# Kernel tuning notes

Measured on AMD Instinct MI355X. Metric: run time of the kernel, lower is better.

The kernel has to match this reference:

```python
import jax, jax.numpy as jnp
import numpy as np

T, N, D = 64, 40, 4
H, R, K = 256, 64, 2
E = N * (N - 1)


def _xavier(key, shape):
    std = (2.0 / (shape[0] + shape[1])) ** 0.5
    return (std * jax.random.normal(key, shape)).astype(jnp.float32)


def setup_inputs() -> dict:
    ks = iter(jax.random.split(jax.random.key(0), 40))
    send, recv = np.where(np.ones((N, N)) - np.eye(N))  # fully-connected directed graph, E = N*(N-1)
    p = {}
    p['inputs'] = jax.random.normal(next(ks), (1, T, N, D), dtype=jnp.float32)
    p['node_masks'] = jnp.ones((1, T, N), dtype=jnp.float32)
    p['send_edges'] = jnp.asarray(send, dtype=jnp.int32)
    p['recv_edges'] = jnp.asarray(recv, dtype=jnp.int32)
    for name, nin in (('mlp1', D), ('mlp2', 2 * H), ('mlp3', H), ('mlp4', 3 * H)):
        p[name + '_W1'] = _xavier(next(ks), (H, nin))
        p[name + '_b1'] = jnp.full((H,), 0.1, jnp.float32)
        p[name + '_W2'] = _xavier(next(ks), (H, H))
        p[name + '_b2'] = jnp.full((H,), 0.1, jnp.float32)
    s = float(1.0 / np.sqrt(R))
    for nm in ('fwd', 'rev'):
        p[nm + '_Wih'] = jax.random.uniform(next(ks), (4 * R, H), jnp.float32, -s, s)
        p[nm + '_Whh'] = jax.random.uniform(next(ks), (4 * R, R), jnp.float32, -s, s)
        p[nm + '_bih'] = jnp.zeros((4 * R,), jnp.float32)
        p[nm + '_bhh'] = jnp.zeros((4 * R,), jnp.float32)
    p['enc_W'] = _xavier(next(ks), (K, 2 * R))
    p['enc_b'] = jnp.full((K,), 0.1, jnp.float32)
    p['prior_W'] = _xavier(next(ks), (K, R))
    p['prior_b'] = jnp.full((K,), 0.1, jnp.float32)
    return p


def _mlp(x, W1, b1, W2, b2):
    # RefNRIMLP in eval mode with no_bn=True: elu(fc2(elu(fc1(x))))
    return jax.nn.elu(jax.nn.elu(x @ W1.T + b1) @ W2.T + b2)


def _lstm(xs, Wih, Whh, bih, bhh):
    # xs: [T, E, H] -> hidden states [T, E, R]; PyTorch LSTM gate order i, f, g, o
    def step(carry, xt):
        h, c = carry
        g = xt @ Wih.T + bih + h @ Whh.T + bhh
        i, f, gg, o = jnp.split(g, 4, axis=-1)
        c = jax.nn.sigmoid(f) * c + jax.nn.sigmoid(i) * jnp.tanh(gg)
        h = jax.nn.sigmoid(o) * jnp.tanh(c)
        return (h, c), h
    Rh = Whh.shape[1]
    init = (jnp.zeros((xs.shape[1], Rh), xs.dtype), jnp.zeros((xs.shape[1], Rh), xs.dtype))
    _, hs = jax.lax.scan(step, init, xs)
    return hs


def _encode(inputs, send, recv,
            m1W1, m1b1, m1W2, m1b2, m2W1, m2b1, m2W2, m2b2,
            m3W1, m3b1, m3W2, m3b2, m4W1, m4b1, m4W2, m4b2,
            fWih, fWhh, fbih, fbhh, rWih, rWhh, rbih, rbhh,
            encW, encb, priW, prib):
    x = inputs[0]                                                  # [T, N, D]
    h = _mlp(x, m1W1, m1b1, m1W2, m1b2)                            # [T, N, H]
    e = jnp.concatenate([h[:, send], h[:, recv]], axis=-1)         # node2edge gather [T, E, 2H]
    e = _mlp(e, m2W1, m2b1, m2W2, m2b2)                            # [T, E, H]
    skip = e
    n = jnp.zeros((x.shape[0], x.shape[1], e.shape[-1]), e.dtype)
    n = n.at[:, recv].add(e)                                       # edge2node scatter-add (index_add_)
    n = _mlp(n, m3W1, m3b1, m3W2, m3b2)                            # [T, N, H]
    e = jnp.concatenate([n[:, send], n[:, recv], skip], axis=-1)   # [T, E, 3H]
    e = _mlp(e, m4W1, m4b1, m4W2, m4b2)                            # per-edge features over time [T, E, H]
    fwd_h = _lstm(e, fWih, fWhh, fbih, fbhh)                       # [T, E, R]
    rev_h = _lstm(e[::-1], rWih, rWhh, rbih, rbhh)[::-1]           # [T, E, R]
    prior = fwd_h @ priW.T + prib                                  # [T, E, K]
    enc = jnp.concatenate([fwd_h, rev_h], axis=-1) @ encW.T + encb # [T, E, K]
    return jnp.concatenate([prior, enc], axis=-1)                  # [T, E, 2K]


def reference(inputs, node_masks, send_edges, recv_edges,
              mlp1_W1, mlp1_b1, mlp1_W2, mlp1_b2,
              mlp2_W1, mlp2_b1, mlp2_W2, mlp2_b2,
              mlp3_W1, mlp3_b1, mlp3_W2, mlp3_b2,
              mlp4_W1, mlp4_b1, mlp4_W2, mlp4_b2,
              fwd_Wih, fwd_Whh, fwd_bih, fwd_bhh,
              rev_Wih, rev_Whh, rev_bih, rev_bhh,
              enc_W, enc_b, prior_W, prior_b):
    del node_masks  # all nodes present -> static fully-connected graph each step
    return _encode(inputs, send_edges, recv_edges,
                   mlp1_W1, mlp1_b1, mlp1_W2, mlp1_b2,
                   mlp2_W1, mlp2_b1, mlp2_W2, mlp2_b2,
                   mlp3_W1, mlp3_b1, mlp3_W2, mlp3_b2,
                   mlp4_W1, mlp4_b1, mlp4_W2, mlp4_b2,
                   fwd_Wih, fwd_Whh, fwd_bih, fwd_bhh,
                   rev_Wih, rev_Whh, rev_bih, rev_bhh,
                   enc_W, enc_b, prior_W, prior_b)
```

## Files before the change

kernel.cpp:

```cpp
#include <hip/hip_runtime.h>
#include <math.h>

#define T_ 64
#define N_ 40
#define D_ 4
#define H_ 256
#define R_ 64
#define E_ 1560
#define TE_ (T_*E_)
#define TN_ (T_*N_)

typedef unsigned short us;
typedef short short8 __attribute__((ext_vector_type(8)));
typedef float f32x4 __attribute__((ext_vector_type(4)));

__device__ __forceinline__ float elu_f(float x){ return x > 0.f ? x : (__expf(x) - 1.f); }
__device__ __forceinline__ float sig_f(float x){ return 1.f/(1.f+__expf(-x)); }
__device__ __forceinline__ float tanh_f(float x){ return 2.f/(1.f+__expf(-2.f*x)) - 1.f; }
__device__ __forceinline__ float dot4(float4 a, float4 b){ return a.x*b.x + a.y*b.y + a.z*b.z + a.w*b.w; }

__device__ __forceinline__ float bf2f(us u){ return __uint_as_float(((unsigned int)u) << 16); }
__device__ __forceinline__ us f2bf(float f){
    unsigned int u = __float_as_uint(f);
    u += 0x7FFFu + ((u >> 16) & 1u);
    return (us)(u >> 16);
}
__device__ __forceinline__ float4 ld4f(const float* p){ return *(const float4*)p; }
__device__ __forceinline__ float4 ld4f(const us* p){
    ushort4 v = *(const ushort4*)p;
    return make_float4(bf2f(v.x), bf2f(v.y), bf2f(v.z), bf2f(v.w));
}
__device__ __forceinline__ void st4f(float* p, float4 v){ *(float4*)p = v; }
__device__ __forceinline__ void st4f(us* p, float4 v){
    ushort4 o; o.x = f2bf(v.x); o.y = f2bf(v.y); o.z = f2bf(v.z); o.w = f2bf(v.w);
    *(ushort4*)p = o;
}

__device__ __forceinline__ void gld16(void* lds, const void* g){
    __builtin_amdgcn_global_load_lds((const __attribute__((address_space(1))) unsigned int*)g,
                                     (__attribute__((address_space(3))) unsigned int*)lds,
                                     16, 0, 0);
}

__device__ __forceinline__ void wsplit1(const float* W, us* hi, us* lo, int i){
    const float w = W[i];
    const us h = f2bf(w);
    hi[i] = h;
    lo[i] = f2bf(w - bf2f(h));
}

__device__ __forceinline__ void wsplitF(const float* __restrict__ W, int stride, int colOff,
                                        us* hi, us* lo, int i){
    const int jj   = i & 7;
    const int lane = (i >> 3) & 63;
    const int mt   = (i >> 9) & 1;
    const int k    = (i >> 10) & 7;
    const int fh   = i >> 13;
    const int R = fh * 32 + mt * 16 + (lane & 15);
    const int K = k * 32 + (lane >> 4) * 8 + jj;
    const float w = W[(size_t)R * stride + colOff + K];
    const us h = f2bf(w);
    hi[i] = h;
    lo[i] = f2bf(w - bf2f(h));
}

__global__ __launch_bounds__(256)
void wsplit_all(const float* __restrict__ s0, us* h0, us* l0,
                const float* __restrict__ s1, us* h1, us* l1,
                const float* __restrict__ s2, us* h2, us* l2,
                const float* __restrict__ s3, us* h3, us* l3,
                const float* __restrict__ s4, us* h4, us* l4,
                const float* __restrict__ s5, us* h5, us* l5,
                const float* __restrict__ s6, us* h6, us* l6)
{
    int i = blockIdx.x * 256 + threadIdx.x;
    if (i < 65536) { wsplitF(s0, 256,   0, h0, l0, i); return; } i -= 65536;
    if (i < 65536) { wsplitF(s1, 768, 512, h1, l1, i); return; } i -= 65536;
    if (i < 65536) { wsplitF(s2, 256,   0, h2, l2, i); return; } i -= 65536;
    if (i < 65536) { wsplitF(s3, 256,   0, h3, l3, i); return; } i -= 65536;
    if (i < 65536) { wsplitF(s4, 256,   0, h4, l4, i); return; } i -= 65536;
    if (i < 16384) { wsplit1(s5, h5, l5, i); return; } i -= 16384;
    wsplit1(s6, h6, l6, i);
}

__global__ __launch_bounds__(256)
void mlp1_kernel(const float* __restrict__ x,
                 const float* __restrict__ W1, const float* __restrict__ b1,
                 const float* __restrict__ W2, const float* __restrict__ b2,
                 us* __restrict__ hout)
{
    __shared__ float xs[8][4];
    __shared__ float h1[8][256];
    const int tid = threadIdx.x;
    const int r0  = blockIdx.x * 8;

    if (tid < 32) xs[tid >> 2][tid & 3] = x[r0 * 4 + tid];
    __syncthreads();

    const float4 w1 = *(const float4*)&W1[tid * 4];
    const float bb1 = b1[tid];
    #pragma unroll
    for (int row = 0; row < 8; ++row) {
        float v = bb1 + xs[row][0]*w1.x + xs[row][1]*w1.y + xs[row][2]*w1.z + xs[row][3]*w1.w;
        h1[row][tid] = elu_f(v);
    }
    __syncthreads();

    float acc[8];
    const float bb2 = b2[tid];
    #pragma unroll
    for (int row = 0; row < 8; ++row) acc[row] = bb2;
    const float* w2row = W2 + (size_t)tid * 256;
    for (int k4 = 0; k4 < 64; ++k4) {
        const float4 w = *(const float4*)&w2row[k4 * 4];
        #pragma unroll
        for (int row = 0; row < 8; ++row) {
            const float4 hh = *(const float4*)&h1[row][k4 * 4];
            acc[row] += dot4(hh, w);
        }
    }
    #pragma unroll
    for (int row = 0; row < 8; ++row)
        hout[(size_t)(r0 + row) * 256 + tid] = f2bf(elu_f(acc[row]));
}

__global__ __launch_bounds__(256)
void node_proj(const us* __restrict__ A, const float* __restrict__ W,
               int wstride, float* __restrict__ P)
{
    __shared__ float As[16][64];
    __shared__ float Ws[16][64];

    const int tid  = threadIdx.x;
    const int am   = tid >> 2;
    const int gm   = blockIdx.x * 64 + am;
    const int part = blockIdx.y >> 2;
    const int wq   = blockIdx.y & 3;

    const us* aptr = A + (size_t)gm * 256;
    const float* wptr = W + (size_t)(wq * 64 + am) * wstride + part * 256;

    const int tx = tid & 15, ty = tid >> 4;
    float acc[4][4] = {};

    for (int k0 = 0; k0 < 256; k0 += 16) {
        const float4 a4 = ld4f(aptr + k0 + (tid & 3) * 4);
        const float4 w4 = *(const float4*)(wptr + k0 + (tid & 3) * 4);

        __syncthreads();
        const int ak = (tid & 3) * 4;
        As[ak+0][am] = a4.x; As[ak+1][am] = a4.y; As[ak+2][am] = a4.z; As[ak+3][am] = a4.w;
        Ws[ak+0][am] = w4.x; Ws[ak+1][am] = w4.y; Ws[ak+2][am] = w4.z; Ws[ak+3][am] = w4.w;
        __syncthreads();

        #pragma unroll
        for (int kq = 0; kq < 16; ++kq) {
            const float4 av = *(const float4*)&As[kq][ty * 4];
            const float4 wv = *(const float4*)&Ws[kq][tx * 4];
            const float a_[4] = {av.x, av.y, av.z, av.w};
            const float w_[4] = {wv.x, wv.y, wv.z, wv.w};
            #pragma unroll
            for (int i = 0; i < 4; ++i)
                #pragma unroll
                for (int j = 0; j < 4; ++j)
                    acc[i][j] += a_[i] * w_[j];
        }
    }

    const int gn = part * 256 + wq * 64 + tx * 4;
    #pragma unroll
    for (int i = 0; i < 4; ++i) {
        const int row = blockIdx.x * 64 + ty * 4 + i;
        float4 o;
        o.x = acc[i][0]; o.y = acc[i][1]; o.z = acc[i][2]; o.w = acc[i][3];
        *(float4*)(P + (size_t)row * 512 + gn) = o;
    }
}

__global__ __launch_bounds__(256)
void edge_gather_elu(const float* __restrict__ P, const float* __restrict__ b1,
                     const int* __restrict__ send, const int* __restrict__ recv,
                     us* __restrict__ out)
{
    const int tid = threadIdx.x;
    const int r   = blockIdx.x * 4 + (tid >> 6);
    const int c4  = (tid & 63) * 4;
    const int t = r / E_;
    const int e = r - t * E_;
    const float4 a  = *(const float4*)(P + ((size_t)(t * N_ + send[e])) * 512 + c4);
    const float4 b  = *(const float4*)(P + ((size_t)(t * N_ + recv[e])) * 512 + 256 + c4);
    const float4 bb = *(const float4*)(b1 + c4);
    float4 v;
    v.x = elu_f(a.x + b.x + bb.x);
    v.y = elu_f(a.y + b.y + bb.y);
    v.z = elu_f(a.z + b.z + bb.z);
    v.w = elu_f(a.w + b.w + bb.w);
    ushort4 o; o.x = f2bf(v.x); o.y = f2bf(v.y); o.z = f2bf(v.z); o.w = f2bf(v.w);
    *(ushort4*)(out + (size_t)r * 256 + c4) = o;
}

#define VM0   0x3F70

#define GEMM_CORE(WHp, WLp)                                                              \
    {                                                                                    \
        const us* wbh = (WHp) + fh * 8192 + lane * 8;                                    \
        const us* wbl = (WLp) + fh * 8192 + lane * 8;                                    \
        short8 whb[3][2], wlb[3][2];                                                     \
        _Pragma("unroll")                                                                \
        for (int s = 0; s < 2; ++s)                                                      \
            _Pragma("unroll")                                                            \
            for (int mt = 0; mt < 2; ++mt) {                                             \
                whb[s][mt] = *(const short8*)(wbh + (s * 2 + mt) * 512);                 \
                wlb[s][mt] = *(const short8*)(wbl + (s * 2 + mt) * 512);                 \
            }                                                                            \
        _Pragma("unroll")                                                                \
        for (int k = 0; k < 8; ++k) {                                                    \
            const int cs = k % 3, ns = (k + 2) % 3;                                      \
            if (k < 6) {                                                                 \
                _Pragma("unroll")                                                        \
                for (int mt = 0; mt < 2; ++mt) {                                         \
                    whb[ns][mt] = *(const short8*)(wbh + ((k + 2) * 2 + mt) * 512);      \
                    wlb[ns][mt] = *(const short8*)(wbl + ((k + 2) * 2 + mt) * 512);      \
                }                                                                        \
            }                                                                            \
            __builtin_amdgcn_sched_barrier(0);                                           \
            short8 ef[4];                                                                \
            _Pragma("unroll")                                                            \
            for (int nt = 0; nt < 4; ++nt)                                               \
                ef[nt] = *(const short8*)(AG + k * 8192 + (eh * 4 + nt) * 1024           \
                                          + ml * 64 + qs16);                             \
            __builtin_amdgcn_s_setprio(1);                                               \
            _Pragma("unroll")                                                            \
            for (int nt = 0; nt < 4; ++nt)                                               \
                _Pragma("unroll")                                                        \
                for (int mt = 0; mt < 2; ++mt) {                                         \
                    acc[mt][nt] = __builtin_amdgcn_mfma_f32_16x16x32_bf16(               \
                        whb[cs][mt], ef[nt], acc[mt][nt], 0, 0, 0);                      \
                    acc[mt][nt] = __builtin_amdgcn_mfma_f32_16x16x32_bf16(               \
                        wlb[cs][mt], ef[nt], acc[mt][nt], 0, 0, 0);                      \
                }                                                                        \
            __builtin_amdgcn_s_setprio(0);                                               \
            __builtin_amdgcn_sched_barrier(0);                                           \
        }                                                                                \
    }

__global__ __launch_bounds__(1024, 4)
void gemm_bf(const us* __restrict__ A, const us* __restrict__ WH, const us* __restrict__ WL,
             const float* __restrict__ bias, us* __restrict__ C)
{
    __shared__ char AG[65536];

    const int tid = threadIdx.x, lane = tid & 63, w = tid >> 6;
    const int ml = lane & 15, q = lane >> 4;
    const int lr = lane >> 2;
    const int cofs = (((lane & 3) ^ ((lane >> 3) & 3)) * 8);
    const int qs16 = (q ^ ((ml >> 1) & 3)) * 16;
    const int bx = blockIdx.x;
    const int eh = w >> 3;
    const int fh = w & 7;

    {
        const int ks = w >> 1;
        const int gb = (w & 1) * 4;
        #pragma unroll
        for (int i = 0; i < 4; ++i)
            gld16(AG + ks * 8192 + (gb + i) * 1024,
                  A + (size_t)(bx * 128 + (gb + i) * 16 + lr) * 256 + ks * 32 + cofs);
    }
    __builtin_amdgcn_s_waitcnt(VM0);
    __syncthreads();

    f32x4 acc[2][4];
    #pragma unroll
    for (int mt = 0; mt < 2; ++mt)
        #pragma unroll
        for (int nt = 0; nt < 4; ++nt) acc[mt][nt] = (f32x4){0.f,0.f,0.f,0.f};

    GEMM_CORE(WH, WL)

    #pragma unroll
    for (int mt = 0; mt < 2; ++mt) {
        const int col = fh * 32 + mt * 16 + q * 4;
        const float4 bb = *(const float4*)(bias + col);
        #pragma unroll
        for (int nt = 0; nt < 4; ++nt) {
            const int row = bx * 128 + eh * 64 + nt * 16 + ml;
            float4 v;
            v.x = elu_f(acc[mt][nt][0] + bb.x); v.y = elu_f(acc[mt][nt][1] + bb.y);
            v.z = elu_f(acc[mt][nt][2] + bb.z); v.w = elu_f(acc[mt][nt][3] + bb.w);
            ushort4 o; o.x = f2bf(v.x); o.y = f2bf(v.y); o.z = f2bf(v.z); o.w = f2bf(v.w);
            *(ushort4*)(C + (size_t)row * 256 + col) = o;
        }
    }
}

__global__ __launch_bounds__(1024, 4)
void fused_m4(const us* __restrict__ Askip,
              const us* __restrict__ w4aH, const us* __restrict__ w4aL, const float* __restrict__ m4b1,
              const us* __restrict__ w4bH, const us* __restrict__ w4bL, const float* __restrict__ m4b2,
              const us* __restrict__ wfiH, const us* __restrict__ wfiL,
              const float* __restrict__ fbih, const float* __restrict__ fbhh,
              const us* __restrict__ wriH, const us* __restrict__ wriL,
              const float* __restrict__ rbih, const float* __restrict__ rbhh,
              const float* __restrict__ Ptab, const int* __restrict__ send, const int* __restrict__ recv,
              us* __restrict__ Gf, us* __restrict__ Gr)
{
    __shared__ char AG[65536];

    const int tid = threadIdx.x, lane = tid & 63, w = tid >> 6;
    const int ml = lane & 15, q = lane >> 4;
    const int lr = lane >> 2;
    const int cofs = (((lane & 3) ^ ((lane >> 3) & 3)) * 8);
    const int qs16 = (q ^ ((ml >> 1) & 3)) * 16;
    const int bx = blockIdx.x;
    const int eh = w >> 3;
    const int fh = w & 7;

    int gtOf[2];
    #pragma unroll
    for (int mt = 0; mt < 2; ++mt)
        gtOf[mt] = fh * 8192 + ml * 64 + (((mt * 2 + (q >> 1)) ^ ((ml >> 1) & 3)) * 16) + (q & 1) * 8;

    f32x4 acc[2][4];

    {
        const int ks = w >> 1;
        const int gb = (w & 1) * 4;
        #pragma unroll
        for (int i = 0; i < 4; ++i)
            gld16(AG + ks * 8192 + (gb + i) * 1024,
                  Askip + (size_t)(bx * 128 + (gb + i) * 16 + lr) * 256 + ks * 32 + cofs);
    }
    __builtin_amdgcn_s_waitcnt(VM0);
    __syncthreads();

    ushort4 r16[2][4];

    #pragma unroll
    for (int mt = 0; mt < 2; ++mt)
        #pragma unroll
        for (int nt = 0; nt < 4; ++nt) acc[mt][nt] = (f32x4){0.f,0.f,0.f,0.f};
    GEMM_CORE(w4aH, w4aL)
    {
        int srw[4], rrw[4];
        #pragma unroll
        for (int nt = 0; nt < 4; ++nt) {
            const int row = bx * 128 + eh * 64 + nt * 16 + ml;
            const int t = row / E_;
            const int e = row - t * E_;
            srw[nt] = t * N_ + send[e];
            rrw[nt] = t * N_ + recv[e];
        }
        #pragma unroll
        for (int mt = 0; mt < 2; ++mt) {
            const int col = fh * 32 + mt * 16 + q * 4;
            const float4 bb = *(const float4*)(m4b1 + col);
            #pragma unroll
            for (int nt = 0; nt < 4; ++nt) {
                float4 v;
                v.x = acc[mt][nt][0] + bb.x; v.y = acc[mt][nt][1] + bb.y;
                v.z = acc[mt][nt][2] + bb.z; v.w = acc[mt][nt][3] + bb.w;
                const float4 pS = *(const float4*)(Ptab + (size_t)srw[nt] * 512 + col);
                const float4 pR = *(const float4*)(Ptab + (size_t)rrw[nt] * 512 + 256 + col);
                v.x += pS.x + pR.x; v.y += pS.y + pR.y;
                v.z += pS.z + pR.z; v.w += pS.w + pR.w;
                v.x = elu_f(v.x); v.y = elu_f(v.y); v.z = elu_f(v.z); v.w = elu_f(v.w);
                ushort4 o; o.x = f2bf(v.x); o.y = f2bf(v.y); o.z = f2bf(v.z); o.w = f2bf(v.w);
                r16[mt][nt] = o;
            }
        }
    }
    __syncthreads();
    #pragma unroll
    for (int mt = 0; mt < 2; ++mt)
        #pragma unroll
        for (int nt = 0; nt < 4; ++nt)
            *(ushort4*)(AG + gtOf[mt] + (eh * 4 + nt) * 1024) = r16[mt][nt];
    __syncthreads();

    #pragma unroll
    for (int mt = 0; mt < 2; ++mt)
        #pragma unroll
        for (int nt = 0; nt < 4; ++nt) acc[mt][nt] = (f32x4){0.f,0.f,0.f,0.f};
    GEMM_CORE(w4bH, w4bL)
    #pragma unroll
    for (int mt = 0; mt < 2; ++mt) {
        const int col = fh * 32 + mt * 16 + q * 4;
        const float4 bb = *(const float4*)(m4b2 + col);
        #pragma unroll
        for (int nt = 0; nt < 4; ++nt) {
            float4 v;
            v.x = elu_f(acc[mt][nt][0] + bb.x); v.y = elu_f(acc[mt][nt][1] + bb.y);
            v.z = elu_f(acc[mt][nt][2] + bb.z); v.w = elu_f(acc[mt][nt][3] + bb.w);
            ushort4 o; o.x = f2bf(v.x); o.y = f2bf(v.y); o.z = f2bf(v.z); o.w = f2bf(v.w);
            r16[mt][nt] = o;
        }
    }
    __syncthreads();
    #pragma unroll
    for (int mt = 0; mt < 2; ++mt)
        #pragma unroll
        for (int nt = 0; nt < 4; ++nt)
            *(ushort4*)(AG + gtOf[mt] + (eh * 4 + nt) * 1024) = r16[mt][nt];
    __syncthreads();

    #pragma unroll
    for (int mt = 0; mt < 2; ++mt)
        #pragma unroll
        for (int nt = 0; nt < 4; ++nt) acc[mt][nt] = (f32x4){0.f,0.f,0.f,0.f};
    GEMM_CORE(wfiH, wfiL)
    #pragma unroll
    for (int mt = 0; mt < 2; ++mt) {
        const int col = fh * 32 + mt * 16 + q * 4;
        float4 bb = *(const float4*)(fbih + col);
        const float4 b2 = *(const float4*)(fbhh + col);
        bb.x += b2.x; bb.y += b2.y; bb.z += b2.z; bb.w += b2.w;
        #pragma unroll
        for (int nt = 0; nt < 4; ++nt) {
            const int row = bx * 128 + eh * 64 + nt * 16 + ml;
            float4 v;
            v.x = acc[mt][nt][0] + bb.x; v.y = acc[mt][nt][1] + bb.y;
            v.z = acc[mt][nt][2] + bb.z; v.w = acc[mt][nt][3] + bb.w;
            ushort4 o; o.x = f2bf(v.x); o.y = f2bf(v.y); o.z = f2bf(v.z); o.w = f2bf(v.w);
            *(ushort4*)(Gf + (size_t)row * 256 + col) = o;
        }
    }

    #pragma unroll
    for (int mt = 0; mt < 2; ++mt)
        #pragma unroll
        for (int nt = 0; nt < 4; ++nt) acc[mt][nt] = (f32x4){0.f,0.f,0.f,0.f};
    GEMM_CORE(wriH, wriL)
    #pragma unroll
    for (int mt = 0; mt < 2; ++mt) {
        const int col = fh * 32 + mt * 16 + q * 4;
        float4 bb = *(const float4*)(rbih + col);
        const float4 b2 = *(const float4*)(rbhh + col);
        bb.x += b2.x; bb.y += b2.y; bb.z += b2.z; bb.w += b2.w;
        #pragma unroll
        for (int nt = 0; nt < 4; ++nt) {
            const int row = bx * 128 + eh * 64 + nt * 16 + ml;
            float4 v;
            v.x = acc[mt][nt][0] + bb.x; v.y = acc[mt][nt][1] + bb.y;
            v.z = acc[mt][nt][2] + bb.z; v.w = acc[mt][nt][3] + bb.w;
            ushort4 o; o.x = f2bf(v.x); o.y = f2bf(v.y); o.z = f2bf(v.z); o.w = f2bf(v.w);
            *(ushort4*)(Gr + (size_t)row * 256 + col) = o;
        }
    }
}

template<bool DOELU, typename TA, typename TC>
__global__ __launch_bounds__(256)
void gemm_nt(const TA* __restrict__ A, const float* __restrict__ W,
             const float* __restrict__ bias1,
             TC* __restrict__ C, int M, int Kdim)
{
    __shared__ float As[16][64];
    __shared__ float Ws[16][64];

    const int tid = threadIdx.x;
    const int am  = tid >> 2;
    const int ak  = (tid & 3) * 4;
    const int gm  = blockIdx.x * 64 + am;

    const TA* aptr0 = A + (size_t)gm * Kdim;
    const float* wptr = W + (size_t)(blockIdx.y * 64 + am) * Kdim;

    const int tx = tid & 15, ty = tid >> 4;
    float acc[4][4] = {};

    for (int k0 = 0; k0 < Kdim; k0 += 16) {
        const float4 a4 = ld4f(aptr0 + k0 + ak);
        const float4 w4 = *(const float4*)(wptr + k0 + (tid & 3) * 4);

        __syncthreads();
        As[ak+0][am] = a4.x; As[ak+1][am] = a4.y; As[ak+2][am] = a4.z; As[ak+3][am] = a4.w;
        const int wk = (tid & 3) * 4;
        Ws[wk+0][am] = w4.x; Ws[wk+1][am] = w4.y; Ws[wk+2][am] = w4.z; Ws[wk+3][am] = w4.w;
        __syncthreads();

        #pragma unroll
        for (int kq = 0; kq < 16; ++kq) {
            const float4 av = *(const float4*)&As[kq][ty * 4];
            const float4 wv = *(const float4*)&Ws[kq][tx * 4];
            const float a_[4] = {av.x, av.y, av.z, av.w};
            const float w_[4] = {wv.x, wv.y, wv.z, wv.w};
            #pragma unroll
            for (int i = 0; i < 4; ++i)
                #pragma unroll
                for (int j = 0; j < 4; ++j)
                    acc[i][j] += a_[i] * w_[j];
        }
    }

    const int gn = blockIdx.y * 64 + tx * 4;
    const float4 bb = *(const float4*)&bias1[gn];
    #pragma unroll
    for (int i = 0; i < 4; ++i) {
        const int row = blockIdx.x * 64 + ty * 4 + i;
        float4 o;
        o.x = acc[i][0] + bb.x; o.y = acc[i][1] + bb.y;
        o.z = acc[i][2] + bb.z; o.w = acc[i][3] + bb.w;
        if (DOELU) { o.x = elu_f(o.x); o.y = elu_f(o.y); o.z = elu_f(o.z); o.w = elu_f(o.w); }
        st4f(C + (size_t)row * 256 + gn, o);
    }
}

__global__ __launch_bounds__(256)
void aggregate_kernel(const us* __restrict__ eSkip, const int* __restrict__ recv,
                      float* __restrict__ nAgg)
{
    const int t = blockIdx.x / N_;
    const int j = blockIdx.x - t * N_;
    const int c = threadIdx.x;
    const us* basep = eSkip + (size_t)t * E_ * H_ + c;
    float acc = 0.f;
    #pragma unroll
    for (int s = 0; s < N_; ++s) {
        if (s == j) continue;
        const int e = s * (N_ - 1) + (j < s ? j : j - 1);
        acc += bf2f(basep[(size_t)e * H_]);
    }
    nAgg[(size_t)blockIdx.x * H_ + c] = acc;
}

__global__ __launch_bounds__(256)
void lstm_mfma(const us* __restrict__ Gf, const us* __restrict__ Gr,
               const us* __restrict__ fWhhH, const us* __restrict__ fWhhL,
               const us* __restrict__ rWhhH, const us* __restrict__ rWhhL,
               float* __restrict__ hsF, float* __restrict__ hsR)
{
    const int NBD = (E_ + 15) / 16;
    const bool revd = (int)blockIdx.x >= NBD;
    const int blk = revd ? (int)blockIdx.x - NBD : (int)blockIdx.x;
    const int e0 = blk * 16;
    const us* G  = revd ? Gr : Gf;
    const us* WH = revd ? rWhhH : fWhhH;
    const us* WL = revd ? rWhhL : fWhhL;
    float* hs    = revd ? hsR : hsF;

    const int tid  = threadIdx.x;
    const int lane = tid & 63;
    const int w    = tid >> 6;
    const int ml   = lane & 15;
    const int q    = lane >> 4;

    __shared__ us hHi[2][16][72];
    __shared__ us hLo[2][16][72];

    short8 wfh[4][2], wfl[4][2];
    #pragma unroll
    for (int mt = 0; mt < 4; ++mt) {
        const int row = mt * 64 + w * 16 + ml;
        #pragma unroll
        for (int ks = 0; ks < 2; ++ks) {
            wfh[mt][ks] = *(const short8*)(WH + (size_t)row * 64 + ks * 32 + q * 8);
            wfl[mt][ks] = *(const short8*)(WL + (size_t)row * 64 + ks * 32 + q * 8);
        }
    }

    for (int i = tid; i < 16 * 72; i += 256) { (&hHi[0][0][0])[i] = 0; (&hLo[0][0][0])[i] = 0; }

    const int eMF = min(e0 + ml, E_ - 1);
    const bool wr = (e0 + ml) < E_;
    const int gOfs = w * 16 + q * 4;
    float4 cst = make_float4(0.f, 0.f, 0.f, 0.f);

    ushort4 gcur[4], gnxt[4];
    {
        const int tt0 = revd ? (T_ - 1) : 0;
        const us* gp = G + ((size_t)tt0 * E_ + eMF) * 256 + gOfs;
        #pragma unroll
        for (int mt = 0; mt < 4; ++mt) gcur[mt] = *(const ushort4*)(gp + mt * 64);
    }
    __syncthreads();

    for (int s = 0; s < T_; ++s) {
        const int tt = revd ? (T_ - 1 - s) : s;
        {
            const int sn = (s + 1 < T_) ? s + 1 : s;
            const int tn = revd ? (T_ - 1 - sn) : sn;
            const us* gp = G + ((size_t)tn * E_ + eMF) * 256 + gOfs;
            #pragma unroll
            for (int mt = 0; mt < 4; ++mt) gnxt[mt] = *(const ushort4*)(gp + mt * 64);
        }
        const int rb = s & 1, wb = rb ^ 1;
        short8 bh[2], bl[2];
        #pragma unroll
        for (int ks = 0; ks < 2; ++ks) {
            bh[ks] = *(const short8*)(&hHi[rb][ml][ks * 32 + q * 8]);
            bl[ks] = *(const short8*)(&hLo[rb][ml][ks * 32 + q * 8]);
        }
        f32x4 acc[4];
        #pragma unroll
        for (int mt = 0; mt < 4; ++mt) {
            acc[mt][0] = bf2f(gcur[mt].x); acc[mt][1] = bf2f(gcur[mt].y);
            acc[mt][2] = bf2f(gcur[mt].z); acc[mt][3] = bf2f(gcur[mt].w);
            #pragma unroll
            for (int ks = 0; ks < 2; ++ks) {
                acc[mt] = __builtin_amdgcn_mfma_f32_16x16x32_bf16(wfh[mt][ks], bh[ks], acc[mt], 0, 0, 0);
                acc[mt] = __builtin_amdgcn_mfma_f32_16x16x32_bf16(wfh[mt][ks], bl[ks], acc[mt], 0, 0, 0);
                acc[mt] = __builtin_amdgcn_mfma_f32_16x16x32_bf16(wfl[mt][ks], bh[ks], acc[mt], 0, 0, 0);
            }
        }
        float4 hv;
        cst.x = sig_f(acc[1][0])*cst.x + sig_f(acc[0][0])*tanh_f(acc[2][0]); hv.x = sig_f(acc[3][0])*tanh_f(cst.x);
        cst.y = sig_f(acc[1][1])*cst.y + sig_f(acc[0][1])*tanh_f(acc[2][1]); hv.y = sig_f(acc[3][1])*tanh_f(cst.y);
        cst.z = sig_f(acc[1][2])*cst.z + sig_f(acc[0][2])*tanh_f(acc[2][2]); hv.z = sig_f(acc[3][2])*tanh_f(cst.z);
        cst.w = sig_f(acc[1][3])*cst.w + sig_f(acc[0][3])*tanh_f(acc[2][3]); hv.w = sig_f(acc[3][3])*tanh_f(cst.w);
        ushort4 hh4, hl4;
        hh4.x = f2bf(hv.x); hl4.x = f2bf(hv.x - bf2f(hh4.x));
        hh4.y = f2bf(hv.y); hl4.y = f2bf(hv.y - bf2f(hh4.y));
        hh4.z = f2bf(hv.z); hl4.z = f2bf(hv.z - bf2f(hh4.z));
        hh4.w = f2bf(hv.w); hl4.w = f2bf(hv.w - bf2f(hh4.w));
        *(ushort4*)(&hHi[wb][ml][gOfs]) = hh4;
        *(ushort4*)(&hLo[wb][ml][gOfs]) = hl4;
        if (wr)
            *(float4*)(&hs[((size_t)tt * E_ + e0 + ml) * 64 + gOfs]) = hv;
        __syncthreads();
        #pragma unroll
        for (int mt = 0; mt < 4; ++mt) gcur[mt] = gnxt[mt];
    }
}

__global__ __launch_bounds__(256)
void out_kernel(const float* __restrict__ hsF, const float* __restrict__ hsR,
                const float* __restrict__ priW, const float* __restrict__ prib,
                const float* __restrict__ encW, const float* __restrict__ encb,
                float* __restrict__ out)
{
    const int idx = blockIdx.x * 256 + threadIdx.x;
    const float* f = hsF + (size_t)idx * 64;
    const float* r = hsR + (size_t)idx * 64;
    float p0 = prib[0], p1 = prib[1], q0 = encb[0], q1 = encb[1];
    #pragma unroll
    for (int k4 = 0; k4 < 16; ++k4) {
        const float4 fv = *(const float4*)(f + k4 * 4);
        const float4 rv = *(const float4*)(r + k4 * 4);
        p0 += dot4(fv, *(const float4*)(priW + k4 * 4));
        p1 += dot4(fv, *(const float4*)(priW + 64 + k4 * 4));
        q0 += dot4(fv, *(const float4*)(encW + k4 * 4))
            + dot4(rv, *(const float4*)(encW + 64 + k4 * 4));
        q1 += dot4(fv, *(const float4*)(encW + 128 + k4 * 4))
            + dot4(rv, *(const float4*)(encW + 192 + k4 * 4));
    }
    float4 o; o.x = p0; o.y = p1; o.z = q0; o.w = q1;
    *(float4*)(out + (size_t)idx * 4) = o;
}

extern "C" void kernel_launch(void* const* d_in, const int* in_sizes, int n_in,
                              void* d_out, int out_size, void* d_ws, size_t ws_size,
                              hipStream_t stream)
{
    const float* x    = (const float*)d_in[0];
    const int*   send = (const int*)d_in[2];
    const int*   recv = (const int*)d_in[3];
    const float* m1W1 = (const float*)d_in[4];  const float* m1b1 = (const float*)d_in[5];
    const float* m1W2 = (const float*)d_in[6];  const float* m1b2 = (const float*)d_in[7];
    const float* m2W1 = (const float*)d_in[8];  const float* m2b1 = (const float*)d_in[9];
    const float* m2W2 = (const float*)d_in[10]; const float* m2b2 = (const float*)d_in[11];
    const float* m3W1 = (const float*)d_in[12]; const float* m3b1 = (const float*)d_in[13];
    const float* m3W2 = (const float*)d_in[14]; const float* m3b2 = (const float*)d_in[15];
    const float* m4W1 = (const float*)d_in[16]; const float* m4b1 = (const float*)d_in[17];
    const float* m4W2 = (const float*)d_in[18]; const float* m4b2 = (const float*)d_in[19];
    const float* fWih = (const float*)d_in[20]; const float* fWhh = (const float*)d_in[21];
    const float* fbih = (const float*)d_in[22]; const float* fbhh = (const float*)d_in[23];
    const float* rWih = (const float*)d_in[24]; const float* rWhh = (const float*)d_in[25];
    const float* rbih = (const float*)d_in[26]; const float* rbhh = (const float*)d_in[27];
    const float* encW = (const float*)d_in[28]; const float* encb = (const float*)d_in[29];
    const float* priW = (const float*)d_in[30]; const float* prib = (const float*)d_in[31];

    const size_t SZN  = (size_t)TN_ * H_;
    const size_t SZE  = (size_t)TE_ * H_;
    float* n_agg = (float*)d_ws;
    float* m3t   = n_agg + SZN;
    float* Ptab  = (float*)d_ws;
    us* h16      = (us*)(m3t + SZN);
    us* n3       = h16 + SZN;
    us* w2bH = n3  + SZN;          us* w2bL = w2bH + 65536;
    us* w4aH = w2bL + 65536;       us* w4aL = w4aH + 65536;
    us* w4bH = w4aL + 65536;       us* w4bL = w4bH + 65536;
    us* wfiH = w4bL + 65536;       us* wfiL = wfiH + 65536;
    us* wriH = wfiL + 65536;       us* wriL = wriH + 65536;
    us* whfH = wriL + 65536;       us* whfL = whfH + 16384;
    us* whrH = whfL + 16384;       us* whrL = whrH + 16384;
    us* bufA16 = whrL + 16384;
    us* bufB16 = bufA16 + SZE;
    us* bufC16 = bufB16 + SZE;
    float* hsF = (float*)bufC16;
    float* hsR = hsF + (size_t)TE_ * R_;
    const size_t needed = ((size_t)(bufC16 + SZE) - (size_t)d_ws);
    if (ws_size < needed) return;

    const dim3 gN(TN_ / 64, 4), gNP(TN_ / 64, 8);

    wsplit_all<<<1408, 256, 0, stream>>>(m2W2, w2bH, w2bL,
                                         m4W1, w4aH, w4aL,
                                         m4W2, w4bH, w4bL,
                                         fWih, wfiH, wfiL, rWih, wriH, wriL,
                                         fWhh, whfH, whfL, rWhh, whrH, whrL);

    mlp1_kernel<<<TN_ / 8, 256, 0, stream>>>(x, m1W1, m1b1, m1W2, m1b2, h16);
    node_proj<<<gNP, 256, 0, stream>>>(h16, m2W1, 512, Ptab);
    edge_gather_elu<<<TE_ / 4, 256, 0, stream>>>(Ptab, m2b1, send, recv, bufA16);
    gemm_bf<<<TE_ / 128, 1024, 0, stream>>>(bufA16, w2bH, w2bL, m2b2, bufB16);
    aggregate_kernel<<<TN_, 256, 0, stream>>>(bufB16, recv, n_agg);
    gemm_nt<true, float, float><<<gN, 256, 0, stream>>>(n_agg, m3W1, m3b1, m3t, TN_, 256);
    gemm_nt<true, float, us><<<gN, 256, 0, stream>>>(m3t, m3W2, m3b2, n3, TN_, 256);
    node_proj<<<gNP, 256, 0, stream>>>(n3, m4W1, 768, Ptab);
    fused_m4<<<TE_ / 128, 1024, 0, stream>>>(bufB16,
                                             w4aH, w4aL, m4b1,
                                             w4bH, w4bL, m4b2,
                                             wfiH, wfiL, fbih, fbhh,
                                             wriH, wriL, rbih, rbhh,
                                             Ptab, send, recv, bufA16, bufB16);
    lstm_mfma<<<2 * ((E_ + 15) / 16), 256, 0, stream>>>(bufA16, bufB16, whfH, whfL, whrH, whrL, hsF, hsR);
    out_kernel<<<TE_ / 256, 256, 0, stream>>>(hsF, hsR, priW, prib, encW, encb, (float*)d_out);
}
```

Baseline: 543.3 us.

## Fuse edge gather+ELU into gemm_bf and shrink MFMA blocks to 64 rows

Removes the standalone edge_gather_elu kernel. gemm_bf now builds its bf16 A tile directly in LDS from the node projection table, which avoids writing and re-reading a TE×256 intermediate through global memory. Both gemm_bf and fused_m4 go from 1024-thread, 128-row blocks to 512-thread, 64-row blocks, halving LDS use and doubling the block count. The software-pipelined triple-buffered weight prefetch is replaced by simple per-k loads, which may expose more load latency.

```diff
diff --git a/kernel.cpp b/kernel.cpp
--- a/kernel.cpp
+++ b/kernel.cpp
@@ -177,97 +177,79 @@
     }
 }
 
-__global__ __launch_bounds__(256)
-void edge_gather_elu(const float* __restrict__ P, const float* __restrict__ b1,
-                     const int* __restrict__ send, const int* __restrict__ recv,
-                     us* __restrict__ out)
-{
-    const int tid = threadIdx.x;
-    const int r   = blockIdx.x * 4 + (tid >> 6);
-    const int c4  = (tid & 63) * 4;
-    const int t = r / E_;
-    const int e = r - t * E_;
-    const float4 a  = *(const float4*)(P + ((size_t)(t * N_ + send[e])) * 512 + c4);
-    const float4 b  = *(const float4*)(P + ((size_t)(t * N_ + recv[e])) * 512 + 256 + c4);
-    const float4 bb = *(const float4*)(b1 + c4);
-    float4 v;
-    v.x = elu_f(a.x + b.x + bb.x);
-    v.y = elu_f(a.y + b.y + bb.y);
-    v.z = elu_f(a.z + b.z + bb.z);
-    v.w = elu_f(a.w + b.w + bb.w);
-    ushort4 o; o.x = f2bf(v.x); o.y = f2bf(v.y); o.z = f2bf(v.z); o.w = f2bf(v.w);
-    *(ushort4*)(out + (size_t)r * 256 + c4) = o;
-}
-
 #define VM0   0x3F70
 
-#define GEMM_CORE(WHp, WLp)                                                              \
+#define GEMM_CORE64(WHp, WLp)                                                            \
     {                                                                                    \
-        const us* wbh = (WHp) + fh * 8192 + lane * 8;                                    \
-        const us* wbl = (WLp) + fh * 8192 + lane * 8;                                    \
-        short8 whb[3][2], wlb[3][2];                                                     \
+        const us* wbh = (WHp) + w * 8192 + lane * 8;                                     \
+        const us* wbl = (WLp) + w * 8192 + lane * 8;                                     \
         _Pragma("unroll")                                                                \
-        for (int s = 0; s < 2; ++s)                                                      \
+        for (int k = 0; k < 8; ++k) {                                                    \
+            short8 wh[2], wl[2], ef[4];                                                  \
             _Pragma("unroll")                                                            \
             for (int mt = 0; mt < 2; ++mt) {                                             \
-                whb[s][mt] = *(const short8*)(wbh + (s * 2 + mt) * 512);                 \
-                wlb[s][mt] = *(const short8*)(wbl + (s * 2 + mt) * 512);                 \
+                wh[mt] = *(const short8*)(wbh + (k * 2 + mt) * 512);                     \
+                wl[mt] = *(const short8*)(wbl + (k * 2 + mt) * 512);                     \
             }                                                                            \
-        _Pragma("unroll")                                                                \
-        for (int k = 0; k < 8; ++k) {                                                    \
-            const int cs = k % 3, ns = (k + 2) % 3;                                      \
-            if (k < 6) {                                                                 \
-                _Pragma("unroll")                                                        \
-                for (int mt = 0; mt < 2; ++mt) {                                         \
-                    whb[ns][mt] = *(const short8*)(wbh + ((k + 2) * 2 + mt) * 512);      \
-                    wlb[ns][mt] = *(const short8*)(wbl + ((k + 2) * 2 + mt) * 512);      \
-                }                                                                        \
-            }                                                                            \
-            __builtin_amdgcn_sched_barrier(0);                                           \
-            short8 ef[4];                                                                \
             _Pragma("unroll")                                                            \
             for (int nt = 0; nt < 4; ++nt)                                               \
-                ef[nt] = *(const short8*)(AG + k * 8192 + (eh * 4 + nt) * 1024           \
-                                          + ml * 64 + qs16);                             \
+                ef[nt] = *(const short8*)(AG + k * 4096 + nt * 1024 + ml * 64 + qs16);   \
             __builtin_amdgcn_s_setprio(1);                                               \
             _Pragma("unroll")                                                            \
             for (int nt = 0; nt < 4; ++nt)                                               \
                 _Pragma("unroll")                                                        \
                 for (int mt = 0; mt < 2; ++mt) {                                         \
                     acc[mt][nt] = __builtin_amdgcn_mfma_f32_16x16x32_bf16(               \
-                        whb[cs][mt], ef[nt], acc[mt][nt], 0, 0, 0);                      \
+                        wh[mt], ef[nt], acc[mt][nt], 0, 0, 0);                           \
                     acc[mt][nt] = __builtin_amdgcn_mfma_f32_16x16x32_bf16(               \
-                        wlb[cs][mt], ef[nt], acc[mt][nt], 0, 0, 0);                      \
+                        wl[mt], ef[nt], acc[mt][nt], 0, 0, 0);                           \
                 }                                                                        \
             __builtin_amdgcn_s_setprio(0);                                               \
-            __builtin_amdgcn_sched_barrier(0);                                           \
         }                                                                                \
     }
 
-__global__ __launch_bounds__(1024, 4)
-void gemm_bf(const us* __restrict__ A, const us* __restrict__ WH, const us* __restrict__ WL,
-             const float* __restrict__ bias, us* __restrict__ C)
-{
-    __shared__ char AG[65536];
+__global__ __launch_bounds__(512, 8)
+void gemm_bf(const float* __restrict__ Ptab, const float* __restrict__ b1,
+             const int* __restrict__ send, const int* __restrict__ recv,
+             const us* __restrict__ WH, const us* __restrict__ WL,
+             const float* __restrict__ bias2, us* __restrict__ C)
+{
+    __shared__ char AG[32768];
 
     const int tid = threadIdx.x, lane = tid & 63, w = tid >> 6;
     const int ml = lane & 15, q = lane >> 4;
-    const int lr = lane >> 2;
-    const int cofs = (((lane & 3) ^ ((lane >> 3) & 3)) * 8);
     const int qs16 = (q ^ ((ml >> 1) & 3)) * 16;
     const int bx = blockIdx.x;
-    const int eh = w >> 3;
-    const int fh = w & 7;
 
     {
-        const int ks = w >> 1;
-        const int gb = (w & 1) * 4;
-        #pragma unroll
-        for (int i = 0; i < 4; ++i)
-            gld16(AG + ks * 8192 + (gb + i) * 1024,
-                  A + (size_t)(bx * 128 + (gb + i) * 16 + lr) * 256 + ks * 32 + cofs);
-    }
-    __builtin_amdgcn_s_waitcnt(VM0);
+        int srw[4], rrw[4];
+        #pragma unroll
+        for (int nt = 0; nt < 4; ++nt) {
+            const int row = bx * 64 + nt * 16 + ml;
+            const int t = row / E_;
+            const int e = row - t * E_;
+            srw[nt] = t * N_ + send[e];
+            rrw[nt] = t * N_ + recv[e];
+        }
+        #pragma unroll
+        for (int mt = 0; mt < 2; ++mt) {
+            const int col = w * 32 + mt * 16 + q * 4;
+            const float4 bb = *(const float4*)(b1 + col);
+            const int of = w * 4096 + ml * 64 + (((mt * 2 + (q >> 1)) ^ ((ml >> 1) & 3)) * 16) + (q & 1) * 8;
+            #pragma unroll
+            for (int nt = 0; nt < 4; ++nt) {
+                const float4 a = *(const float4*)(Ptab + (size_t)srw[nt] * 512 + col);
+                const float4 b = *(const float4*)(Ptab + (size_t)rrw[nt] * 512 + 256 + col);
+                float4 v;
+                v.x = elu_f(a.x + b.x + bb.x);
+                v.y = elu_f(a.y + b.y + bb.y);
+                v.z = elu_f(a.z + b.z + bb.z);
+                v.w = elu_f(a.w + b.w + bb.w);
+                ushort4 o; o.x = f2bf(v.x); o.y = f2bf(v.y); o.z = f2bf(v.z); o.w = f2bf(v.w);
+                *(ushort4*)(AG + of + nt * 1024) = o;
+            }
+        }
+    }
     __syncthreads();
 
     f32x4 acc[2][4];
@@ -276,15 +258,15 @@
         #pragma unroll
         for (int nt = 0; nt < 4; ++nt) acc[mt][nt] = (f32x4){0.f,0.f,0.f,0.f};
 
-    GEMM_CORE(WH, WL)
+    GEMM_CORE64(WH, WL)
 
     #pragma unroll
     for (int mt = 0; mt < 2; ++mt) {
-        const int col = fh * 32 + mt * 16 + q * 4;
-        const float4 bb = *(const float4*)(bias + col);
+        const int col = w * 32 + mt * 16 + q * 4;
+        const float4 bb = *(const float4*)(bias2 + col);
         #pragma unroll
         for (int nt = 0; nt < 4; ++nt) {
-            const int row = bx * 128 + eh * 64 + nt * 16 + ml;
+            const int row = bx * 64 + nt * 16 + ml;
             float4 v;
             v.x = elu_f(acc[mt][nt][0] + bb.x); v.y = elu_f(acc[mt][nt][1] + bb.y);
             v.z = elu_f(acc[mt][nt][2] + bb.z); v.w = elu_f(acc[mt][nt][3] + bb.w);
@@ -294,7 +276,7 @@
     }
 }
 
-__global__ __launch_bounds__(1024, 4)
+__global__ __launch_bounds__(512, 8)
 void fused_m4(const us* __restrict__ Askip,
               const us* __restrict__ w4aH, const us* __restrict__ w4aL, const float* __restrict__ m4b1,
               const us* __restrict__ w4bH, const us* __restrict__ w4bL, const float* __restrict__ m4b2,
@@ -305,7 +287,7 @@
               const float* __restrict__ Ptab, const int* __restrict__ send, const int* __restrict__ recv,
               us* __restrict__ Gf, us* __restrict__ Gr)
 {
-    __shared__ char AG[65536];
+    __shared__ char AG[32768];
 
     const int tid = threadIdx.x, lane = tid & 63, w = tid >> 6;
     const int ml = lane & 15, q = lane >> 4;
@@ -313,24 +295,18 @@
     const int cofs = (((lane & 3) ^ ((lane >> 3) & 3)) * 8);
     const int qs16 = (q ^ ((ml >> 1) & 3)) * 16;
     const int bx = blockIdx.x;
-    const int eh = w >> 3;
-    const int fh = w & 7;
 
     int gtOf[2];
     #pragma unroll
     for (int mt = 0; mt < 2; ++mt)
-        gtOf[mt] = fh * 8192 + ml * 64 + (((mt * 2 + (q >> 1)) ^ ((ml >> 1) & 3)) * 16) + (q & 1) * 8;
+        gtOf[mt] = w * 4096 + ml * 64 + (((mt * 2 + (q >> 1)) ^ ((ml >> 1) & 3)) * 16) + (q & 1) * 8;
 
     f32x4 acc[2][4];
 
-    {
-        const int ks = w >> 1;
-        const int gb = (w & 1) * 4;
-        #pragma unroll
-        for (int i = 0; i < 4; ++i)
-            gld16(AG + ks * 8192 + (gb + i) * 1024,
-                  Askip + (size_t)(bx * 128 + (gb + i) * 16 + lr) * 256 + ks * 32 + cofs);
-    }
+    #pragma unroll
+    for (int g = 0; g < 4; ++g)
+        gld16(AG + w * 4096 + g * 1024,
+              Askip + (size_t)(bx * 64 + g * 16 + lr) * 256 + w * 32 + cofs);
     __builtin_amdgcn_s_waitcnt(VM0);
     __syncthreads();
 
@@ -340,12 +316,12 @@
     for (int mt = 0; mt < 2; ++mt)
         #pragma unroll
         for (int nt = 0; nt < 4; ++nt) acc[mt][nt] = (f32x4){0.f,0.f,0.f,0.f};
-    GEMM_CORE(w4aH, w4aL)
+    GEMM_CORE64(w4aH, w4aL)
     {
         int srw[4], rrw[4];
         #pragma unroll
         for (int nt = 0; nt < 4; ++nt) {
-            const int row = bx * 128 + eh * 64 + nt * 16 + ml;
+            const int row = bx * 64 + nt * 16 + ml;
             const int t = row / E_;
             const int e = row - t * E_;
             srw[nt] = t * N_ + send[e];
@@ -353,7 +329,7 @@
         }
         #pragma unroll
         for (int mt = 0; mt < 2; ++mt) {
-            const int col = fh * 32 + mt * 16 + q * 4;
+            const int col = w * 32 + mt * 16 + q * 4;
             const float4 bb = *(const float4*)(m4b1 + col);
             #pragma unroll
             for (int nt = 0; nt < 4; ++nt) {
@@ -375,17 +351,17 @@
     for (int mt = 0; mt < 2; ++mt)
         #pragma unroll
         for (int nt = 0; nt < 4; ++nt)
-            *(ushort4*)(AG + gtOf[mt] + (eh * 4 + nt) * 1024) = r16[mt][nt];
+            *(ushort4*)(AG + gtOf[mt] + nt * 1024) = r16[mt][nt];
     __syncthreads();
 
     #pragma unroll
     for (int mt = 0; mt < 2; ++mt)
         #pragma unroll
         for (int nt = 0; nt < 4; ++nt) acc[mt][nt] = (f32x4){0.f,0.f,0.f,0.f};
-    GEMM_CORE(w4bH, w4bL)
+    GEMM_CORE64(w4bH, w4bL)
     #pragma unroll
     for (int mt = 0; mt < 2; ++mt) {
-        const int col = fh * 32 + mt * 16 + q * 4;
+        const int col = w * 32 + mt * 16 + q * 4;
         const float4 bb = *(const float4*)(m4b2 + col);
         #pragma unroll
         for (int nt = 0; nt < 4; ++nt) {
@@ -401,23 +377,23 @@
     for (int mt = 0; mt < 2; ++mt)
         #pragma unroll
         for (int nt = 0; nt < 4; ++nt)
-            *(ushort4*)(AG + gtOf[mt] + (eh * 4 + nt) * 1024) = r16[mt][nt];
+            *(ushort4*)(AG + gtOf[mt] + nt * 1024) = r16[mt][nt];
     __syncthreads();
 
     #pragma unroll
     for (int mt = 0; mt < 2; ++mt)
         #pragma unroll
         for (int nt = 0; nt < 4; ++nt) acc[mt][nt] = (f32x4){0.f,0.f,0.f,0.f};
-    GEMM_CORE(wfiH, wfiL)
+    GEMM_CORE64(wfiH, wfiL)
     #pragma unroll
     for (int mt = 0; mt < 2; ++mt) {
-        const int col = fh * 32 + mt * 16 + q * 4;
+        const int col = w * 32 + mt * 16 + q * 4;
         float4 bb = *(const float4*)(fbih + col);
         const float4 b2 = *(const float4*)(fbhh + col);
         bb.x += b2.x; bb.y += b2.y; bb.z += b2.z; bb.w += b2.w;
         #pragma unroll
         for (int nt = 0; nt < 4; ++nt) {
-            const int row = bx * 128 + eh * 64 + nt * 16 + ml;
+            const int row = bx * 64 + nt * 16 + ml;
             float4 v;
             v.x = acc[mt][nt][0] + bb.x; v.y = acc[mt][nt][1] + bb.y;
             v.z = acc[mt][nt][2] + bb.z; v.w = acc[mt][nt][3] + bb.w;
@@ -430,16 +406,16 @@
     for (int mt = 0; mt < 2; ++mt)
         #pragma unroll
         for (int nt = 0; nt < 4; ++nt) acc[mt][nt] = (f32x4){0.f,0.f,0.f,0.f};
-    GEMM_CORE(wriH, wriL)
+    GEMM_CORE64(wriH, wriL)
     #pragma unroll
     for (int mt = 0; mt < 2; ++mt) {
-        const int col = fh * 32 + mt * 16 + q * 4;
+        const int col = w * 32 + mt * 16 + q * 4;
         float4 bb = *(const float4*)(rbih + col);
         const float4 b2 = *(const float4*)(rbhh + col);
         bb.x += b2.x; bb.y += b2.y; bb.z += b2.z; bb.w += b2.w;
         #pragma unroll
         for (int nt = 0; nt < 4; ++nt) {
-            const int row = bx * 128 + eh * 64 + nt * 16 + ml;
+            const int row = bx * 64 + nt * 16 + ml;
             float4 v;
             v.x = acc[mt][nt][0] + bb.x; v.y = acc[mt][nt][1] + bb.y;
             v.z = acc[mt][nt][2] + bb.z; v.w = acc[mt][nt][3] + bb.w;
@@ -702,18 +678,17 @@
 
     mlp1_kernel<<<TN_ / 8, 256, 0, stream>>>(x, m1W1, m1b1, m1W2, m1b2, h16);
     node_proj<<<gNP, 256, 0, stream>>>(h16, m2W1, 512, Ptab);
-    edge_gather_elu<<<TE_ / 4, 256, 0, stream>>>(Ptab, m2b1, send, recv, bufA16);
-    gemm_bf<<<TE_ / 128, 1024, 0, stream>>>(bufA16, w2bH, w2bL, m2b2, bufB16);
+    gemm_bf<<<TE_ / 64, 512, 0, stream>>>(Ptab, m2b1, send, recv, w2bH, w2bL, m2b2, bufB16);
     aggregate_kernel<<<TN_, 256, 0, stream>>>(bufB16, recv, n_agg);
     gemm_nt<true, float, float><<<gN, 256, 0, stream>>>(n_agg, m3W1, m3b1, m3t, TN_, 256);
     gemm_nt<true, float, us><<<gN, 256, 0, stream>>>(m3t, m3W2, m3b2, n3, TN_, 256);
     node_proj<<<gNP, 256, 0, stream>>>(n3, m4W1, 768, Ptab);
-    fused_m4<<<TE_ / 128, 1024, 0, stream>>>(bufB16,
-                                             w4aH, w4aL, m4b1,
-                                             w4bH, w4bL, m4b2,
-                                             wfiH, wfiL, fbih, fbhh,
-                                             wriH, wriL, rbih, rbhh,
-                                             Ptab, send, recv, bufA16, bufB16);
+    fused_m4<<<TE_ / 64, 512, 0, stream>>>(bufB16,
+                                           w4aH, w4aL, m4b1,
+                                           w4bH, w4bL, m4b2,
+                                           wfiH, wfiL, fbih, fbhh,
+                                           wriH, wriL, rbih, rbhh,
+                                           Ptab, send, recv, bufA16, bufB16);
     lstm_mfma<<<2 * ((E_ + 15) / 16), 256, 0, stream>>>(bufA16, bufB16, whfH, whfL, whrH, whrL, hsF, hsR);
     out_kernel<<<TE_ / 256, 256, 0, stream>>>(hsF, hsR, priW, prib, encW, encb, (float*)d_out);
 }
```

After: 834.7 us. 53.6% more time.
